# Optimization experiments

Hardware: AMD Instinct MI355X
Metric: run time of the kernel (lower is better)

Reference implementation:

```python
import jax, jax.numpy as jnp
import numpy as np

N = 4096
IN_F = 512
OUT_F = 512
EDGE_F = 4


def setup_inputs() -> dict:
    key = jax.random.key(0)
    k1, k2, k3, k4, k5 = jax.random.split(key, 5)
    stdv_w = 1.0 / np.sqrt(OUT_F)
    return {
        "input": jax.random.normal(k1, (N, IN_F), dtype=jnp.float32),
        "adj": jnp.zeros((N, N), dtype=jnp.float32),  # unused by forward (kept for signature fidelity)
        "E": jax.random.normal(k2, (N * N, EDGE_F), dtype=jnp.float32),
        "weight": jax.random.uniform(k3, (IN_F, OUT_F), minval=-stdv_w, maxval=stdv_w, dtype=jnp.float32),
        "weight_q": jax.random.uniform(k4, (EDGE_F, 1), minval=-1.0, maxval=1.0, dtype=jnp.float32),
        "bias": jax.random.uniform(k5, (OUT_F,), minval=-stdv_w, maxval=stdv_w, dtype=jnp.float32),
    }


def reference(input, adj, E, weight, weight_q, bias):
    # support = X @ W : [N, out_f]
    support = input @ weight
    # project per-edge features to scalar edge weights, reshape to dense [N, N] adjacency
    A = (E @ weight_q).reshape(input.shape[0], input.shape[0])
    # propagate: A @ support + bias
    return A @ support + bias
```

## Files before the change

kernel.cpp:

```cpp
#include <hip/hip_runtime.h>
#include <hip/hip_bf16.h>
#include <stdint.h>

#define N_NODES 4096
#define INF_ 512
#define OUTF_ 512

typedef unsigned short u16;
typedef __attribute__((ext_vector_type(8))) short bf16x8;
typedef __attribute__((ext_vector_type(4))) float f32x4;

__device__ __forceinline__ u16 f2bf(float f) {
    union { float f; uint32_t u; } v; v.f = f;
    uint32_t u = v.u;
    uint32_t r = u + 0x7FFFu + ((u >> 16) & 1u);
    return (u16)(r >> 16);
}

__device__ __forceinline__ void async16(const void* gsrc, void* ldst) {
    __builtin_amdgcn_global_load_lds(
        (const __attribute__((address_space(1))) unsigned int*)gsrc,
        (__attribute__((address_space(3))) unsigned int*)ldst,
        16, 0, 0);
}

__global__ void prep_kernel(const float4* __restrict__ E4, const float* __restrict__ wq,
                            u16* __restrict__ Abf,
                            const float* __restrict__ X, const float* __restrict__ W,
                            u16* __restrict__ Xbf, u16* __restrict__ WT) {
    const int tid = blockIdx.x * blockDim.x + threadIdx.x;
    const float w0 = wq[0], w1 = wq[1], w2 = wq[2], w3 = wq[3];

    if (tid < N_NODES * INF_) Xbf[tid] = f2bf(X[tid]);
    if (tid < INF_ * OUTF_) {
        int n = tid >> 9, k = tid & 511;
        WT[tid] = f2bf(W[k * OUTF_ + n]);
    }

    const int lane = threadIdx.x & 63;
    const long wave = (long)(tid >> 6);
    const long base = wave * 512;
#pragma unroll
    for (int j = 0; j < 8; ++j) {
        long idx = base + j * 64 + lane;
        float4 e = E4[idx];
        Abf[idx] = f2bf(e.x * w0 + e.y * w1 + e.z * w2 + e.w * w3);
    }
}

template<bool TRANS_OUT, bool PARTIAL>
__global__ __launch_bounds__(256)
void gemm64(const u16* __restrict__ A, const u16* __restrict__ B,
            float* __restrict__ outF, u16* __restrict__ outT,
            const float* __restrict__ bias, int K, int KC) {
    __shared__ u16 As[64][32];
    __shared__ u16 Bs[128][32];

    const int tid  = threadIdx.x;
    const int lane = tid & 63;
    const int w    = tid >> 6;
    const int wr   = w >> 1;
    const int wc   = w & 1;
    const int brow = blockIdx.x * 64;
    const int bcol = blockIdx.y * 128;
    const int kt0  = blockIdx.z * KC;

    f32x4 acc[2][4] = {};

    const int srA = w * 16 + (lane >> 2);
    const int srB = w * 32 + (lane >> 2);
    const int sc  = (lane & 3) * 8;

    for (int kt = kt0; kt < kt0 + KC; kt += 32) {
        __syncthreads();
        async16(&A[(long)(brow + srA) * K + kt + sc],      &As[w * 16][0]);
        async16(&B[(long)(bcol + srB) * K + kt + sc],      &Bs[w * 32][0]);
        async16(&B[(long)(bcol + srB + 16) * K + kt + sc], &Bs[w * 32 + 16][0]);
        __syncthreads();

        bf16x8 af[2], bfr[4];
#pragma unroll
        for (int m = 0; m < 2; ++m)
            af[m] = *(const bf16x8*)&As[wr * 32 + m * 16 + (lane & 15)][(lane >> 4) * 8];
#pragma unroll
        for (int n = 0; n < 4; ++n)
            bfr[n] = *(const bf16x8*)&Bs[wc * 64 + n * 16 + (lane & 15)][(lane >> 4) * 8];
#pragma unroll
        for (int m = 0; m < 2; ++m)
#pragma unroll
            for (int n = 0; n < 4; ++n)
                acc[m][n] = __builtin_amdgcn_mfma_f32_16x16x32_bf16(af[m], bfr[n], acc[m][n], 0, 0, 0);
    }

    float* outP = PARTIAL ? outF + (long)blockIdx.z * (N_NODES * OUTF_) : outF;
#pragma unroll
    for (int m = 0; m < 2; ++m) {
#pragma unroll
        for (int n = 0; n < 4; ++n) {
            int col  = bcol + wc * 64 + n * 16 + (lane & 15);
            int row0 = brow + wr * 32 + m * 16 + (lane >> 4) * 4;
            if (TRANS_OUT) {
#pragma unroll
                for (int r = 0; r < 4; ++r)
                    outT[(long)col * N_NODES + row0 + r] = f2bf(acc[m][n][r]);
            } else if (PARTIAL) {
#pragma unroll
                for (int r = 0; r < 4; ++r)
                    outP[(long)(row0 + r) * OUTF_ + col] = acc[m][n][r];
            } else {
                float bv = bias[col];
#pragma unroll
                for (int r = 0; r < 4; ++r)
                    outF[(long)(row0 + r) * OUTF_ + col] = acc[m][n][r] + bv;
            }
        }
    }
}

__global__ void reduce_kernel(const float4* __restrict__ part, const float4* __restrict__ bias4,
                              float4* __restrict__ out) {
    const int tid = blockIdx.x * blockDim.x + threadIdx.x;
    const long stride4 = (long)N_NODES * OUTF_ / 4;
    float4 a = part[tid];
    float4 b = part[tid + stride4];
    float4 c = part[tid + 2 * stride4];
    float4 d = part[tid + 3 * stride4];
    float4 bv = bias4[tid & (OUTF_ / 4 - 1)];
    float4 o;
    o.x = a.x + b.x + c.x + d.x + bv.x;
    o.y = a.y + b.y + c.y + d.y + bv.y;
    o.z = a.z + b.z + c.z + d.z + bv.z;
    o.w = a.w + b.w + c.w + d.w + bv.w;
    out[tid] = o;
}

extern "C" void kernel_launch(void* const* d_in, const int* in_sizes, int n_in,
                              void* d_out, int out_size, void* d_ws, size_t ws_size,
                              hipStream_t stream) {
    const float* X    = (const float*)d_in[0];
    const float* E    = (const float*)d_in[2];
    const float* W    = (const float*)d_in[3];
    const float* wq   = (const float*)d_in[4];
    const float* bias = (const float*)d_in[5];
    float* out = (float*)d_out;

    char* ws = (char*)d_ws;
    u16*   ST    = (u16*)ws;
    u16*   Abf   = (u16*)(ws + (4l << 20));
    u16*   Xbf   = (u16*)(ws + (36l << 20));
    u16*   WT    = (u16*)(ws + (40l << 20));
    float* parts = (float*)(ws + (41l << 20));

    const bool split = ws_size >= (73ul << 20);

    prep_kernel<<<8192, 256, 0, stream>>>((const float4*)E, wq, Abf, X, W, Xbf, WT);
    gemm64<true, false><<<dim3(64, 4, 1), 256, 0, stream>>>(Xbf, WT, nullptr, ST, nullptr, 512, 512);
    if (split) {
        gemm64<false, true><<<dim3(64, 4, 4), 256, 0, stream>>>(Abf, ST, parts, nullptr, nullptr, 4096, 1024);
        reduce_kernel<<<2048, 256, 0, stream>>>((const float4*)parts, (const float4*)bias, (float4*)out);
    } else {
        gemm64<false, false><<<dim3(64, 4, 1), 256, 0, stream>>>(Abf, ST, out, nullptr, bias, 4096, 4096);
    }
}
```

Measured before the change: 114.5 us.

## Fuse edge projection into propagation GEMM to avoid materializing bf16 adjacency

The per-edge projection E@wq is now computed inside the second GEMM, which writes bf16 A values into a small swizzled LDS tile. This removes the separate write and re-read of the 32 MB bf16 adjacency matrix. The new kernel uses 16-row tiles with support operands loaded directly from global memory, so ST is re-read far more often and relies on cache. The split-K path with reduction is now always used.

```diff
diff --git a/kernel.cpp b/kernel.cpp
--- a/kernel.cpp
+++ b/kernel.cpp
@@ -24,35 +24,20 @@
         16, 0, 0);
 }
 
-__global__ void prep_kernel(const float4* __restrict__ E4, const float* __restrict__ wq,
-                            u16* __restrict__ Abf,
-                            const float* __restrict__ X, const float* __restrict__ W,
-                            u16* __restrict__ Xbf, u16* __restrict__ WT) {
-    const int tid = blockIdx.x * blockDim.x + threadIdx.x;
-    const float w0 = wq[0], w1 = wq[1], w2 = wq[2], w3 = wq[3];
-
+__global__ void convert_kernel(const float* __restrict__ X, const float* __restrict__ W,
+                               u16* __restrict__ Xbf, u16* __restrict__ WT) {
+    int tid = blockIdx.x * blockDim.x + threadIdx.x;
     if (tid < N_NODES * INF_) Xbf[tid] = f2bf(X[tid]);
     if (tid < INF_ * OUTF_) {
         int n = tid >> 9, k = tid & 511;
         WT[tid] = f2bf(W[k * OUTF_ + n]);
     }
-
-    const int lane = threadIdx.x & 63;
-    const long wave = (long)(tid >> 6);
-    const long base = wave * 512;
-#pragma unroll
-    for (int j = 0; j < 8; ++j) {
-        long idx = base + j * 64 + lane;
-        float4 e = E4[idx];
-        Abf[idx] = f2bf(e.x * w0 + e.y * w1 + e.z * w2 + e.w * w3);
-    }
 }
 
-template<bool TRANS_OUT, bool PARTIAL>
 __global__ __launch_bounds__(256)
-void gemm64(const u16* __restrict__ A, const u16* __restrict__ B,
-            float* __restrict__ outF, u16* __restrict__ outT,
-            const float* __restrict__ bias, int K, int KC) {
+void gemm_support(const u16* __restrict__ A, const u16* __restrict__ B,
+                  u16* __restrict__ outT) {
+    const int K = 512;
     __shared__ u16 As[64][32];
     __shared__ u16 Bs[128][32];
 
@@ -63,7 +48,6 @@
     const int wc   = w & 1;
     const int brow = blockIdx.x * 64;
     const int bcol = blockIdx.y * 128;
-    const int kt0  = blockIdx.z * KC;
 
     f32x4 acc[2][4] = {};
 
@@ -71,7 +55,7 @@
     const int srB = w * 32 + (lane >> 2);
     const int sc  = (lane & 3) * 8;
 
-    for (int kt = kt0; kt < kt0 + KC; kt += 32) {
+    for (int kt = 0; kt < K; kt += 32) {
         __syncthreads();
         async16(&A[(long)(brow + srA) * K + kt + sc],      &As[w * 16][0]);
         async16(&B[(long)(bcol + srB) * K + kt + sc],      &Bs[w * 32][0]);
@@ -92,28 +76,73 @@
                 acc[m][n] = __builtin_amdgcn_mfma_f32_16x16x32_bf16(af[m], bfr[n], acc[m][n], 0, 0, 0);
     }
 
-    float* outP = PARTIAL ? outF + (long)blockIdx.z * (N_NODES * OUTF_) : outF;
 #pragma unroll
-    for (int m = 0; m < 2; ++m) {
+    for (int m = 0; m < 2; ++m)
 #pragma unroll
         for (int n = 0; n < 4; ++n) {
             int col  = bcol + wc * 64 + n * 16 + (lane & 15);
             int row0 = brow + wr * 32 + m * 16 + (lane >> 4) * 4;
-            if (TRANS_OUT) {
 #pragma unroll
-                for (int r = 0; r < 4; ++r)
-                    outT[(long)col * N_NODES + row0 + r] = f2bf(acc[m][n][r]);
-            } else if (PARTIAL) {
+            for (int r = 0; r < 4; ++r)
+                outT[(long)col * N_NODES + row0 + r] = f2bf(acc[m][n][r]);
+        }
+}
+
+__global__ __launch_bounds__(512, 6)
+void fused_gemm2(const float4* __restrict__ E4, const float* __restrict__ wq,
+                 const u16* __restrict__ ST, float* __restrict__ parts) {
+    __shared__ u16 As[16 * 32];
+
+    const int tid   = threadIdx.x;
+    const int lane  = tid & 63;
+    const int w     = tid >> 6;
+    const int brow  = blockIdx.x * 16;
+    const int kt0   = blockIdx.y << 10;
+    const int nbase = w * 64;
+
+    const float w0 = wq[0], w1 = wq[1], w2 = wq[2], w3 = wq[3];
+
+    const int srow  = tid >> 5;
+    const int sk    = tid & 31;
+    const int a_off = srow * 64 + (((sk >> 3) ^ ((srow >> 1) & 3)) << 4) + (sk & 7) * 2;
+    const float4* eptr = E4 + (long)(brow + srow) * N_NODES + kt0 + sk;
+
+    const int ar   = lane & 15;
+    const int ahi  = lane >> 4;
+    const int qsw  = ahi ^ ((ar >> 1) & 3);
+    const int a_rd = (ar * 4 + qsw) * 16;
+
+    const u16* bbase[4];
 #pragma unroll
-                for (int r = 0; r < 4; ++r)
-                    outP[(long)(row0 + r) * OUTF_ + col] = acc[m][n][r];
-            } else {
-                float bv = bias[col];
+    for (int n = 0; n < 4; ++n)
+        bbase[n] = ST + (long)(nbase + n * 16 + ar) * N_NODES + kt0 + ahi * 8;
+
+    f32x4 acc[4] = {};
+    float4 ecur = eptr[0];
+
+    for (int s = 0; s < 32; ++s) {
+        __syncthreads();
+        float a = ecur.x * w0 + ecur.y * w1 + ecur.z * w2 + ecur.w * w3;
+        *(u16*)((char*)As + a_off) = f2bf(a);
+        if (s + 1 < 32) ecur = eptr[(s + 1) * 32];
+        bf16x8 bfr[4];
 #pragma unroll
-                for (int r = 0; r < 4; ++r)
-                    outF[(long)(row0 + r) * OUTF_ + col] = acc[m][n][r] + bv;
-            }
-        }
+        for (int n = 0; n < 4; ++n)
+            bfr[n] = *(const bf16x8*)(bbase[n] + s * 32);
+        __syncthreads();
+        bf16x8 af = *(const bf16x8*)((const char*)As + a_rd);
+#pragma unroll
+        for (int n = 0; n < 4; ++n)
+            acc[n] = __builtin_amdgcn_mfma_f32_16x16x32_bf16(af, bfr[n], acc[n], 0, 0, 0);
+    }
+
+    float* outP = parts + (long)blockIdx.y * (N_NODES * OUTF_);
+#pragma unroll
+    for (int n = 0; n < 4; ++n) {
+        int col = nbase + n * 16 + ar;
+#pragma unroll
+        for (int r = 0; r < 4; ++r)
+            outP[(long)(brow + ahi * 4 + r) * OUTF_ + col] = acc[n][r];
     }
 }
 
@@ -146,19 +175,12 @@
 
     char* ws = (char*)d_ws;
     u16*   ST    = (u16*)ws;
-    u16*   Abf   = (u16*)(ws + (4l << 20));
-    u16*   Xbf   = (u16*)(ws + (36l << 20));
-    u16*   WT    = (u16*)(ws + (40l << 20));
-    float* parts = (float*)(ws + (41l << 20));
+    u16*   Xbf   = (u16*)(ws + (4l << 20));
+    u16*   WT    = (u16*)(ws + (8l << 20));
+    float* parts = (float*)(ws + (9l << 20));
 
-    const bool split = ws_size >= (73ul << 20);
-
-    prep_kernel<<<8192, 256, 0, stream>>>((const float4*)E, wq, Abf, X, W, Xbf, WT);
-    gemm64<true, false><<<dim3(64, 4, 1), 256, 0, stream>>>(Xbf, WT, nullptr, ST, nullptr, 512, 512);
-    if (split) {
-        gemm64<false, true><<<dim3(64, 4, 4), 256, 0, stream>>>(Abf, ST, parts, nullptr, nullptr, 4096, 1024);
-        reduce_kernel<<<2048, 256, 0, stream>>>((const float4*)parts, (const float4*)bias, (float4*)out);
-    } else {
-        gemm64<false, false><<<dim3(64, 4, 1), 256, 0, stream>>>(Abf, ST, out, nullptr, bias, 4096, 4096);
-    }
+    convert_kernel<<<8192, 256, 0, stream>>>(X, W, Xbf, WT);
+    gemm_support<<<dim3(64, 4), 256, 0, stream>>>(Xbf, WT, ST);
+    fused_gemm2<<<dim3(256, 4), 512, 0, stream>>>((const float4*)E, wq, ST, parts);
+    reduce_kernel<<<2048, 256, 0, stream>>>((const float4*)parts, (const float4*)bias, (float4*)out);
 }
```

Result: slower. 185.3 us (+61.8%).
